# Kernel optimization log

Hardware: AMD Instinct MI355X
Metric: run time of the kernel (lower is better)

Reference implementation:

```python
import jax, jax.numpy as jnp
import numpy as np

N = 4096      # nodes
FEAT = 512    # feature_size
HID = 256     # hidden_dim
E = 131072    # edges (avg degree 32)


def setup_inputs() -> dict:
    key = jax.random.key(0)
    ks = jax.random.split(key, 10)
    x = jax.random.normal(ks[0], (N, FEAT), dtype=jnp.float32)
    edge_index = jax.random.randint(ks[1], (2, E), 0, N)
    edge_attr = jax.random.uniform(ks[2], (E, 1), dtype=jnp.float32)
    # nn.Linear(bias=False) weights, stored as [in, out] so k = x @ Wk
    Wk = jax.random.normal(ks[3], (FEAT, HID), dtype=jnp.float32) / np.sqrt(FEAT)
    Wq = jax.random.normal(ks[4], (FEAT, HID), dtype=jnp.float32) / np.sqrt(FEAT)
    Wv = jax.random.normal(ks[5], (FEAT, FEAT), dtype=jnp.float32) / np.sqrt(FEAT)
    # EmbeddingTable.reset_parameters: normal(0, 1), shape [num_embeddings=2, dim]
    Ek = jax.random.normal(ks[6], (2, HID), dtype=jnp.float32)
    Eq = jax.random.normal(ks[7], (2, HID), dtype=jnp.float32)
    Ev = jax.random.normal(ks[8], (2, FEAT), dtype=jnp.float32)
    # ContinuousEmbeddingIndex params
    idx_bias = jnp.full((1,), 0.5, dtype=jnp.float32)
    idx_mult = jnp.full((1,), 10.0, dtype=jnp.float32)
    return dict(x=x, edge_index=edge_index, edge_attr=edge_attr,
                Wk=Wk, Wq=Wq, Wv=Wv, Ek=Ek, Eq=Eq, Ev=Ev,
                idx_bias=idx_bias, idx_mult=idx_mult)


def reference(x, edge_index, edge_attr, Wk, Wq, Wv, Ek, Eq, Ev, idx_bias, idx_mult):
    n = x.shape[0]
    L = x.shape[-1]  # feature_size, used as softmax scale
    src, dst = edge_index[0], edge_index[1]

    # ContinuousEmbeddingIndex: soft 2-way interpolation weights [E, 2]
    s = jax.nn.sigmoid((edge_attr - idx_bias) * idx_mult)
    w = jnp.concatenate([s, 1.0 - s], axis=-1)

    # per-edge relative embeddings (EmbeddingTable: weights @ embeddings)
    rk = w @ Ek   # [E, HID]
    rq = w @ Eq   # [E, HID]
    rv = w @ Ev   # [E, FEAT]

    k = x @ Wk    # [N, HID]
    q = x @ Wq    # [N, HID]
    v = x @ Wv    # [N, FEAT]

    # A = q k^T + (q_i . Rk_ij) + (k_j . Rq_ij) + q k^T
    # The Rk/Rq terms are nonzero only on edges -> compute per-edge and scatter-add
    # (to_dense_adj sums duplicate edges, matched by .add).
    A = 2.0 * (q @ k.T)                                   # [N, N]
    edge_bias = jnp.sum(q[src] * rk, axis=-1) + jnp.sum(k[dst] * rq, axis=-1)  # [E]
    A = A.at[src, dst].add(edge_bias)
    A = jax.nn.softmax(A / np.sqrt(L), axis=-1)           # dropout = identity (eval)

    # M = A v + sum_j A_ij * Rv_ij  (second term only nonzero on edges)
    M = A @ v
    M = M + jax.ops.segment_sum(A[src, dst][:, None] * rv, src, num_segments=n)
    return M
```

## Files before the change

kernel.cpp:

```cpp
#include <hip/hip_runtime.h>
#include <hip/hip_bf16.h>
#include <cmath>


typedef short bf16x8 __attribute__((ext_vector_type(8)));
typedef float f32x4  __attribute__((ext_vector_type(4)));
typedef unsigned short ushort_t;
typedef unsigned short ushort4v __attribute__((ext_vector_type(4)));
typedef unsigned short ushort8v __attribute__((ext_vector_type(8)));

__device__ __forceinline__ ushort_t f2bf(float f) {
    union { float f; unsigned u; } v; v.f = f;
    unsigned u = v.u;
    u += 0x7FFFu + ((u >> 16) & 1u);
    return (ushort_t)(u >> 16);
}
__device__ __forceinline__ float bf2f(ushort_t h) {
    union { unsigned u; float f; } v; v.u = ((unsigned)h) << 16;
    return v.f;
}
__device__ __forceinline__ void gload_lds16(const void* g, void* l) {
    __builtin_amdgcn_global_load_lds(
        (const __attribute__((address_space(1))) void*)g,
        (__attribute__((address_space(3))) void*)l, 16, 0, 0);
}

__device__ __forceinline__ void gemm_core(
    const ushort_t* __restrict__ A, const ushort_t* __restrict__ B,
    int lda, int ldb, int Ksz, size_t kbase, int bm, int bn,
    ushort_t* As, ushort_t* Bs, f32x4 (&acc)[4][4])
{
    constexpr int BK = 32;
    const int tid  = threadIdx.x;
    const int lane = tid & 63;
    const int wid  = tid >> 6;
    const int wm = (wid >> 1) * 64;
    const int wn = (wid & 1) * 64;

    const int r0 = tid >> 2;
    const int c8 = (tid & 3) * 8;
    const ushort_t* Ag0 = A + (size_t)(bm + r0) * lda + kbase + c8;
    const ushort_t* Bg0 = B + (size_t)(bn + r0) * ldb + kbase + c8;
    const ushort_t* Ag1 = Ag0 + (size_t)64 * lda;
    const ushort_t* Bg1 = Bg0 + (size_t)64 * ldb;
    ushort_t* AsW0 = &As[(wid * 64) * 8];
    ushort_t* AsW1 = &As[(256 + wid * 64) * 8];
    ushort_t* BsW0 = &Bs[(wid * 64) * 8];
    ushort_t* BsW1 = &Bs[(256 + wid * 64) * 8];

    const int fr = lane & 15;
    const int kh = (lane >> 4) * 8;

    for (int k0 = 0; k0 < Ksz; k0 += BK) {
        gload_lds16(Ag0 + k0, AsW0);
        gload_lds16(Ag1 + k0, AsW1);
        gload_lds16(Bg0 + k0, BsW0);
        gload_lds16(Bg1 + k0, BsW1);
        __syncthreads();

        bf16x8 af[4], bfv[4];
        #pragma unroll
        for (int i = 0; i < 4; ++i) {
            af[i]  = *(const bf16x8*)&As[(wm + i * 16 + fr) * 32 + kh];
            bfv[i] = *(const bf16x8*)&Bs[(wn + i * 16 + fr) * 32 + kh];
        }
        #pragma unroll
        for (int i = 0; i < 4; ++i)
            #pragma unroll
            for (int j = 0; j < 4; ++j)
                acc[i][j] = __builtin_amdgcn_mfma_f32_16x16x32_bf16(
                    af[i], bfv[j], acc[i][j], 0, 0, 0);
        __syncthreads();
    }
}

__device__ __forceinline__ int swizzle_bid()
{
    int bid = blockIdx.y * gridDim.x + blockIdx.x;
    const int nwg = gridDim.x * gridDim.y;
    if ((nwg & 7) == 0) {
        const int cpx = nwg >> 3;
        bid = (bid & 7) * cpx + (bid >> 3);
    }
    return bid;
}

template<bool STORE_BF16>
__global__ __launch_bounds__(256) void gemm_nt_mfma(
    const ushort_t* __restrict__ A, const ushort_t* __restrict__ B,
    void* __restrict__ Cv, int lda, int ldb, int ldc, int Ksz, float alpha)
{
    __shared__ ushort_t As[128 * 32];
    __shared__ ushort_t Bs[128 * 32];
    const int bid = swizzle_bid();
    const int bm = (bid / gridDim.x) * 128;
    const int bn = (bid % gridDim.x) * 128;
    f32x4 acc[4][4] = {};
    gemm_core(A, B, lda, ldb, Ksz, 0, bm, bn, As, Bs, acc);

    const int lane = threadIdx.x & 63;
    const int wid  = threadIdx.x >> 6;
    const int wm = (wid >> 1) * 64, wn = (wid & 1) * 64;
    const int cr = (lane >> 4) * 4, cc = lane & 15;
    #pragma unroll
    for (int i = 0; i < 4; ++i)
        #pragma unroll
        for (int j = 0; j < 4; ++j) {
            const int col = bn + wn + j * 16 + cc;
            const int rowb = bm + wm + i * 16 + cr;
            #pragma unroll
            for (int jj = 0; jj < 4; ++jj) {
                const float val = alpha * acc[i][j][jj];
                if (STORE_BF16)
                    ((ushort_t*)Cv)[(size_t)(rowb + jj) * ldc + col] = f2bf(val);
                else
                    ((float*)Cv)[(size_t)(rowb + jj) * ldc + col] = val;
            }
        }
}

__global__ __launch_bounds__(256) void proj_gemm(
    const ushort_t* __restrict__ xb, const ushort_t* __restrict__ Wqkt,
    const ushort_t* __restrict__ Wvt, ushort_t* __restrict__ qkb,
    ushort_t* __restrict__ vTb, int FEAT, int HID, int N)
{
    __shared__ ushort_t As[128 * 32];
    __shared__ ushort_t Bs[128 * 32];
    const int b = blockIdx.x;
    const ushort_t* A; const ushort_t* B; ushort_t* C;
    int bm, bn, ldc;
    if (b < 128) {
        const int gx = (2 * HID) / 128;
        bm = (b / gx) * 128; bn = (b % gx) * 128;
        A = xb; B = Wqkt; C = qkb; ldc = 2 * HID;
    } else {
        const int b2 = b - 128;
        const int gx = N / 128;
        bm = (b2 / gx) * 128; bn = (b2 % gx) * 128;
        A = Wvt; B = xb; C = vTb; ldc = N;
    }
    f32x4 acc[4][4] = {};
    gemm_core(A, B, FEAT, FEAT, FEAT, 0, bm, bn, As, Bs, acc);

    const int lane = threadIdx.x & 63;
    const int wid  = threadIdx.x >> 6;
    const int wm = (wid >> 1) * 64, wn = (wid & 1) * 64;
    const int cr = (lane >> 4) * 4, cc = lane & 15;
    #pragma unroll
    for (int i = 0; i < 4; ++i)
        #pragma unroll
        for (int j = 0; j < 4; ++j) {
            const int col = bn + wn + j * 16 + cc;
            const int rowb = bm + wm + i * 16 + cr;
            #pragma unroll
            for (int jj = 0; jj < 4; ++jj)
                C[(size_t)(rowb + jj) * ldc + col] = f2bf(acc[i][j][jj]);
        }
}

__global__ __launch_bounds__(256) void pv_gemm_splitk(
    const ushort_t* __restrict__ P, const ushort_t* __restrict__ vT,
    ushort_t* __restrict__ parts, int N, int FEAT, int Kchunk)
{
    __shared__ ushort_t As[128 * 32];
    __shared__ ushort_t Bs[128 * 32];
    const int bid = swizzle_bid();
    const int bm = (bid / gridDim.x) * 128;
    const int bn = (bid % gridDim.x) * 128;

    f32x4 acc[4][4] = {};
    gemm_core(P, vT, N, N, Kchunk, (size_t)blockIdx.z * Kchunk, bm, bn, As, Bs, acc);

    const int tid = threadIdx.x;
    const int lane = tid & 63;
    const int wid  = tid >> 6;
    const int wm = (wid >> 1) * 64, wn = (wid & 1) * 64;
    const int cr = (lane >> 4) * 4, cc = lane & 15;
    ushort_t* myPart = parts + (size_t)blockIdx.z * N * FEAT;
    #pragma unroll
    for (int i = 0; i < 4; ++i)
        #pragma unroll
        for (int j = 0; j < 4; ++j) {
            const int col = bn + wn + j * 16 + cc;
            const int rowb = bm + wm + i * 16 + cr;
            #pragma unroll
            for (int jj = 0; jj < 4; ++jj)
                myPart[(size_t)(rowb + jj) * FEAT + col] = f2bf(acc[i][j][jj]);
        }
}

__global__ void reduce_add_rv_kernel(
    const ushort_t* __restrict__ parts, float* __restrict__ out,
    const float* __restrict__ c0, const float* __restrict__ c1,
    const float* __restrict__ Ev, int FEAT, size_t zstride, int nz)
{
    const int i8 = blockIdx.x * 256 + threadIdx.x;
    const int F8 = FEAT / 8;
    const int node = i8 / F8;
    const int f0 = (i8 % F8) * 8;
    float s[8] = {};
    for (int z = 0; z < nz; ++z) {
        const ushort8v p = *(const ushort8v*)(parts + (size_t)z * zstride + (size_t)i8 * 8);
        #pragma unroll
        for (int j = 0; j < 8; ++j) s[j] += bf2f(p[j]);
    }
    const float a0 = c0[node], a1 = c1[node];
    float4 o0, o1;
    const float4 e00 = *(const float4*)(Ev + f0);
    const float4 e01 = *(const float4*)(Ev + f0 + 4);
    const float4 e10 = *(const float4*)(Ev + FEAT + f0);
    const float4 e11 = *(const float4*)(Ev + FEAT + f0 + 4);
    o0.x = s[0] + a0 * e00.x + a1 * e10.x;
    o0.y = s[1] + a0 * e00.y + a1 * e10.y;
    o0.z = s[2] + a0 * e00.z + a1 * e10.z;
    o0.w = s[3] + a0 * e00.w + a1 * e10.w;
    o1.x = s[4] + a0 * e01.x + a1 * e11.x;
    o1.y = s[5] + a0 * e01.y + a1 * e11.y;
    o1.z = s[6] + a0 * e01.z + a1 * e11.z;
    o1.w = s[7] + a0 * e01.w + a1 * e11.w;
    float* op = out + (size_t)node * FEAT + f0;
    *(float4*)op = o0;
    *(float4*)(op + 4) = o1;
}

__global__ __launch_bounds__(256) void prep_kernel(
    const float* __restrict__ x, const float* __restrict__ Wq,
    const float* __restrict__ Wk, const float* __restrict__ Wv,
    ushort_t* __restrict__ xb, ushort_t* __restrict__ Wqkt,
    ushort_t* __restrict__ Wvt, int N, int FEAT, int HID)
{
    const int b = blockIdx.x;
    const int tid = threadIdx.x;
    const int xBlocks = (N * FEAT / 8) / 256;
    if (b < xBlocks) {
        const int i = b * 256 + tid;
        const float4 a = ((const float4*)x)[2 * i];
        const float4 c = ((const float4*)x)[2 * i + 1];
        ushort8v o;
        o[0] = f2bf(a.x); o[1] = f2bf(a.y); o[2] = f2bf(a.z); o[3] = f2bf(a.w);
        o[4] = f2bf(c.x); o[5] = f2bf(c.y); o[6] = f2bf(c.z); o[7] = f2bf(c.w);
        ((ushort8v*)xb)[i] = o;
        return;
    }

    __shared__ float tile[32][33];
    const int qkTiles = (FEAT / 32) * (HID / 32);
    int t = b - xBlocks;
    const float* src; ushort_t* dst; int I, O;
    if (t < qkTiles)            { src = Wq; dst = Wqkt;                       I = FEAT; O = HID; }
    else if (t < 2 * qkTiles)   { src = Wk; dst = Wqkt + (size_t)HID * FEAT;  I = FEAT; O = HID; t -= qkTiles; }
    else                        { src = Wv; dst = Wvt;                        I = FEAT; O = FEAT; t -= 2 * qkTiles; }
    const int ot = O / 32;
    const int r0 = (t / ot) * 32;
    const int c0 = (t % ot) * 32;
    const int lr = tid >> 5;
    const int lc = tid & 31;
    #pragma unroll
    for (int rr = 0; rr < 32; rr += 8)
        tile[lr + rr][lc] = src[(size_t)(r0 + lr + rr) * O + c0 + lc];
    __syncthreads();
    #pragma unroll
    for (int rr = 0; rr < 32; rr += 8)
        dst[(size_t)(c0 + lr + rr) * I + r0 + lc] = f2bf(tile[lc][lr + rr]);
}

__global__ __launch_bounds__(256) void node_dots(
    const ushort_t* __restrict__ qk,
    const float* __restrict__ Ek, const float* __restrict__ Eq,
    float* qk0, float* qk1, float* kq0, float* kq1,
    float* c0, float* c1, int HID)
{
    const int node = blockIdx.x;
    const int t = threadIdx.x;
    const ushort_t* row = qk + (size_t)node * (2 * HID);
    const float qv = bf2f(row[t]);
    const float kv = bf2f(row[HID + t]);
    float p0 = qv * Ek[t];
    float p1 = qv * Ek[HID + t];
    float p2 = kv * Eq[t];
    float p3 = kv * Eq[HID + t];
    #pragma unroll
    for (int off = 32; off > 0; off >>= 1) {
        p0 += __shfl_down(p0, off);
        p1 += __shfl_down(p1, off);
        p2 += __shfl_down(p2, off);
        p3 += __shfl_down(p3, off);
    }
    __shared__ float red[4][4];
    if ((t & 63) == 0) {
        const int w = t >> 6;
        red[w][0] = p0; red[w][1] = p1; red[w][2] = p2; red[w][3] = p3;
    }
    __syncthreads();
    if (t == 0) {
        qk0[node] = red[0][0] + red[1][0] + red[2][0] + red[3][0];
        qk1[node] = red[0][1] + red[1][1] + red[2][1] + red[3][1];
        kq0[node] = red[0][2] + red[1][2] + red[2][2] + red[3][2];
        kq1[node] = red[0][3] + red[1][3] + red[2][3] + red[3][3];
        c0[node] = 0.f;
        c1[node] = 0.f;
    }
}

__global__ void edge_bias_kernel(
    const int* __restrict__ ei, const float* __restrict__ attr,
    const float* __restrict__ qk0, const float* __restrict__ qk1,
    const float* __restrict__ kq0, const float* __restrict__ kq1,
    float* __restrict__ A, int E, int N,
    const float* __restrict__ ibp, const float* __restrict__ imp)
{
    const int e = blockIdx.x * blockDim.x + threadIdx.x;
    if (e >= E) return;
    const int src = ei[e];
    const int dst = ei[E + e];
    const float s = 1.f / (1.f + __expf(-(attr[e] - ibp[0]) * imp[0]));
    const float bias = s * qk0[src] + (1.f - s) * qk1[src]
                     + s * kq0[dst] + (1.f - s) * kq1[dst];
    atomicAdd(&A[(size_t)src * N + dst], bias);
}

__global__ __launch_bounds__(256) void softmax_rows_bf16(
    const float* __restrict__ A, ushort_t* __restrict__ P, int N, float scale)
{
    const int row = blockIdx.x;
    const float* a = A + (size_t)row * N;
    ushort_t* p = P + (size_t)row * N;
    const int t = threadIdx.x;
    float4 vals[4];
    float mx = -1e30f;
    #pragma unroll
    for (int u = 0; u < 4; ++u) {
        float4 vv = ((const float4*)a)[t + u * 256];
        vv.x *= scale; vv.y *= scale; vv.z *= scale; vv.w *= scale;
        vals[u] = vv;
        mx = fmaxf(mx, fmaxf(fmaxf(vv.x, vv.y), fmaxf(vv.z, vv.w)));
    }
    __shared__ float red[4];
    #pragma unroll
    for (int off = 32; off > 0; off >>= 1) mx = fmaxf(mx, __shfl_down(mx, off));
    if ((t & 63) == 0) red[t >> 6] = mx;
    __syncthreads();
    const float m = fmaxf(fmaxf(red[0], red[1]), fmaxf(red[2], red[3]));
    __syncthreads();
    float sum = 0.f;
    #pragma unroll
    for (int u = 0; u < 4; ++u) {
        vals[u].x = __expf(vals[u].x - m);
        vals[u].y = __expf(vals[u].y - m);
        vals[u].z = __expf(vals[u].z - m);
        vals[u].w = __expf(vals[u].w - m);
        sum += vals[u].x + vals[u].y + vals[u].z + vals[u].w;
    }
    #pragma unroll
    for (int off = 32; off > 0; off >>= 1) sum += __shfl_down(sum, off);
    if ((t & 63) == 0) red[t >> 6] = sum;
    __syncthreads();
    const float inv = 1.f / (red[0] + red[1] + red[2] + red[3]);
    #pragma unroll
    for (int u = 0; u < 4; ++u) {
        ushort4v o;
        o[0] = f2bf(vals[u].x * inv);
        o[1] = f2bf(vals[u].y * inv);
        o[2] = f2bf(vals[u].z * inv);
        o[3] = f2bf(vals[u].w * inv);
        ((ushort4v*)p)[t + u * 256] = o;
    }
}

__global__ void edge_coeff_kernel(
    const int* __restrict__ ei, const float* __restrict__ attr,
    const ushort_t* __restrict__ P, float* __restrict__ c0, float* __restrict__ c1,
    int E, int N, const float* __restrict__ ibp, const float* __restrict__ imp)
{
    const int e = blockIdx.x * blockDim.x + threadIdx.x;
    if (e >= E) return;
    const int src = ei[e];
    const int dst = ei[E + e];
    const float s = 1.f / (1.f + __expf(-(attr[e] - ibp[0]) * imp[0]));
    const float pv = bf2f(P[(size_t)src * N + dst]);
    atomicAdd(&c0[src], pv * s);
    atomicAdd(&c1[src], pv * (1.f - s));
}

extern "C" void kernel_launch(void* const* d_in, const int* in_sizes, int n_in,
                              void* d_out, int out_size, void* d_ws, size_t ws_size,
                              hipStream_t stream)
{
    const float* x    = (const float*)d_in[0];
    const int*   ei   = (const int*)d_in[1];
    const float* attr = (const float*)d_in[2];
    const float* Wk   = (const float*)d_in[3];
    const float* Wq   = (const float*)d_in[4];
    const float* Wv   = (const float*)d_in[5];
    const float* Ek   = (const float*)d_in[6];
    const float* Eq   = (const float*)d_in[7];
    const float* Ev   = (const float*)d_in[8];
    const float* ib   = (const float*)d_in[9];
    const float* im   = (const float*)d_in[10];
    float* out = (float*)d_out;

    const int FEAT = (int)lroundf(sqrtf((float)in_sizes[5]));
    const int HID  = in_sizes[3] / FEAT;
    const int N    = in_sizes[0] / FEAT;
    const int E    = in_sizes[2];

    char* w = (char*)d_ws;
    size_t o = 0;
    ushort_t* xb   = (ushort_t*)(w + o); o += (size_t)N * FEAT * 2;
    ushort_t* Wqkt = (ushort_t*)(w + o); o += (size_t)2 * HID * FEAT * 2;
    ushort_t* Wvt  = (ushort_t*)(w + o); o += (size_t)FEAT * FEAT * 2;
    ushort_t* qkb  = (ushort_t*)(w + o); o += (size_t)N * 2 * HID * 2;
    ushort_t* vTb  = (ushort_t*)(w + o); o += (size_t)FEAT * N * 2;
    float*    Abuf = (float*)(w + o);    o += (size_t)N * N * 4;
    ushort_t* Pb   = (ushort_t*)(w + o); o += (size_t)N * N * 2;
    float*    qk0  = (float*)(w + o);    o += (size_t)N * 4;
    float*    qk1  = (float*)(w + o);    o += (size_t)N * 4;
    float*    kq0  = (float*)(w + o);    o += (size_t)N * 4;
    float*    kq1  = (float*)(w + o);    o += (size_t)N * 4;
    float*    c0   = (float*)(w + o);    o += (size_t)N * 4;
    float*    c1   = (float*)(w + o);    o += (size_t)N * 4;
    ushort_t* pvpart = (ushort_t*)Abuf;

    const dim3 blk(256);
    const int NZ = 4;
    const int Kchunk = N / NZ;

    const int xBlocks = (N * FEAT / 8) / 256;
    const int qkTiles = (FEAT / 32) * (HID / 32);
    const int vTiles  = (FEAT / 32) * (FEAT / 32);
    prep_kernel<<<xBlocks + 2 * qkTiles + vTiles, blk, 0, stream>>>(
        x, Wq, Wk, Wv, xb, Wqkt, Wvt, N, FEAT, HID);

    proj_gemm<<<256, blk, 0, stream>>>(xb, Wqkt, Wvt, qkb, vTb, FEAT, HID, N);

    node_dots<<<N, blk, 0, stream>>>(qkb, Ek, Eq, qk0, qk1, kq0, kq1, c0, c1, HID);

    gemm_nt_mfma<false><<<dim3(N / 128, N / 128), blk, 0, stream>>>(
        qkb, qkb + HID, Abuf, 2 * HID, 2 * HID, N, HID, 2.f);

    edge_bias_kernel<<<(E + 255) / 256, blk, 0, stream>>>(ei, attr, qk0, qk1, kq0, kq1,
                                                          Abuf, E, N, ib, im);

    softmax_rows_bf16<<<N, blk, 0, stream>>>(Abuf, Pb, N, 1.f / sqrtf((float)FEAT));

    edge_coeff_kernel<<<(E + 255) / 256, blk, 0, stream>>>(ei, attr, Pb, c0, c1, E, N, ib, im);

    pv_gemm_splitk<<<dim3(FEAT / 128, N / 128, NZ), blk, 0, stream>>>(
        Pb, vTb, pvpart, N, FEAT, Kchunk);

    reduce_add_rv_kernel<<<(N * FEAT / 8) / 256, blk, 0, stream>>>(
        pvpart, out, c0, c1, Ev, FEAT, (size_t)N * FEAT, NZ);
}
```

Before: 130.9 us.

## Store score matrix in fp16 and apply edge biases via CSR in softmax

The QK^T GEMM now writes pre-scaled fp16 scores instead of fp32, halving the N×N intermediate traffic. Edge biases are no longer atomically added into the dense matrix. Instead, edges are bucketed by source row through a count, a single-block scan and a scatter into CSR order, and the softmax kernel adds them into an LDS copy of the row. This trades a few extra small kernels and LDS atomics for fewer global random atomics and less dense read/write bandwidth, at the cost of fp16 precision on the scores.

```diff
diff --git a/kernel.cpp b/kernel.cpp
--- a/kernel.cpp
+++ b/kernel.cpp
@@ -18,6 +18,12 @@
 __device__ __forceinline__ float bf2f(ushort_t h) {
     union { unsigned u; float f; } v; v.u = ((unsigned)h) << 16;
     return v.f;
+}
+__device__ __forceinline__ ushort_t f2h(float f) {
+    union { _Float16 h; ushort_t u; } v; v.h = (_Float16)f; return v.u;
+}
+__device__ __forceinline__ float h2f(ushort_t u) {
+    union { ushort_t u; _Float16 h; } v; v.u = u; return (float)v.h;
 }
 __device__ __forceinline__ void gload_lds16(const void* g, void* l) {
     __builtin_amdgcn_global_load_lds(
@@ -85,7 +91,7 @@
     return bid;
 }
 
-template<bool STORE_BF16>
+template<int MODE>
 __global__ __launch_bounds__(256) void gemm_nt_mfma(
     const ushort_t* __restrict__ A, const ushort_t* __restrict__ B,
     void* __restrict__ Cv, int lda, int ldb, int ldc, int Ksz, float alpha)
@@ -111,10 +117,12 @@
             #pragma unroll
             for (int jj = 0; jj < 4; ++jj) {
                 const float val = alpha * acc[i][j][jj];
-                if (STORE_BF16)
+                if (MODE == 0)
+                    ((float*)Cv)[(size_t)(rowb + jj) * ldc + col] = val;
+                else if (MODE == 1)
                     ((ushort_t*)Cv)[(size_t)(rowb + jj) * ldc + col] = f2bf(val);
                 else
-                    ((float*)Cv)[(size_t)(rowb + jj) * ldc + col] = val;
+                    ((ushort_t*)Cv)[(size_t)(rowb + jj) * ldc + col] = f2h(val);
             }
         }
 }
@@ -122,11 +130,17 @@
 __global__ __launch_bounds__(256) void proj_gemm(
     const ushort_t* __restrict__ xb, const ushort_t* __restrict__ Wqkt,
     const ushort_t* __restrict__ Wvt, ushort_t* __restrict__ qkb,
-    ushort_t* __restrict__ vTb, int FEAT, int HID, int N)
-{
+    ushort_t* __restrict__ vTb, const int* __restrict__ ei,
+    int* __restrict__ rowcnt, int E, int FEAT, int HID, int N)
+{
+    const int b = blockIdx.x;
+    if (b >= 256) {
+        const int e = (b - 256) * 256 + threadIdx.x;
+        if (e < E) atomicAdd(&rowcnt[ei[e]], 1);
+        return;
+    }
     __shared__ ushort_t As[128 * 32];
     __shared__ ushort_t Bs[128 * 32];
-    const int b = blockIdx.x;
     const ushort_t* A; const ushort_t* B; ushort_t* C;
     int bm, bn, ldc;
     if (b < 128) {
@@ -227,11 +241,21 @@
     const float* __restrict__ x, const float* __restrict__ Wq,
     const float* __restrict__ Wk, const float* __restrict__ Wv,
     ushort_t* __restrict__ xb, ushort_t* __restrict__ Wqkt,
-    ushort_t* __restrict__ Wvt, int N, int FEAT, int HID)
+    ushort_t* __restrict__ Wvt, int* __restrict__ rowcnt,
+    int N, int FEAT, int HID)
 {
     const int b = blockIdx.x;
     const int tid = threadIdx.x;
     const int xBlocks = (N * FEAT / 8) / 256;
+    const int qkTiles = (FEAT / 32) * (HID / 32);
+    const int vTiles  = (FEAT / 32) * (FEAT / 32);
+    const int zBase = xBlocks + 2 * qkTiles + vTiles;
+
+    if (b >= zBase) {
+        const int i = (b - zBase) * 256 + tid;
+        if (i < N) rowcnt[i] = 0;
+        return;
+    }
     if (b < xBlocks) {
         const int i = b * 256 + tid;
         const float4 a = ((const float4*)x)[2 * i];
@@ -244,7 +268,6 @@
     }
 
     __shared__ float tile[32][33];
-    const int qkTiles = (FEAT / 32) * (HID / 32);
     int t = b - xBlocks;
     const float* src; ushort_t* dst; int I, O;
     if (t < qkTiles)            { src = Wq; dst = Wqkt;                       I = FEAT; O = HID; }
@@ -302,69 +325,99 @@
     }
 }
 
-__global__ void edge_bias_kernel(
+__global__ __launch_bounds__(256) void scan_kernel(
+    const int* __restrict__ cnt, int* __restrict__ rowptr,
+    int* __restrict__ rowcur, int N)
+{
+    __shared__ int psum[256];
+    const int t = threadIdx.x;
+    const int per = N / 256;
+    int local[16];
+    int base = 0;
+    for (int i = 0; i < per; ++i) { local[i] = base; base += cnt[t * per + i]; }
+    psum[t] = base;
+    __syncthreads();
+    for (int off = 1; off < 256; off <<= 1) {
+        const int v = (t >= off) ? psum[t - off] : 0;
+        __syncthreads();
+        psum[t] += v;
+        __syncthreads();
+    }
+    const int pre = (t == 0) ? 0 : psum[t - 1];
+    for (int i = 0; i < per; ++i) {
+        rowptr[t * per + i] = pre + local[i];
+        rowcur[t * per + i] = pre + local[i];
+    }
+    if (t == 255) rowptr[N] = psum[255];
+}
+
+__global__ void scatter_kernel(
     const int* __restrict__ ei, const float* __restrict__ attr,
     const float* __restrict__ qk0, const float* __restrict__ qk1,
     const float* __restrict__ kq0, const float* __restrict__ kq1,
-    float* __restrict__ A, int E, int N,
+    int* __restrict__ rowcur, int2* __restrict__ ebuf, int E, float scale,
     const float* __restrict__ ibp, const float* __restrict__ imp)
 {
-    const int e = blockIdx.x * blockDim.x + threadIdx.x;
+    const int e = blockIdx.x * 256 + threadIdx.x;
     if (e >= E) return;
     const int src = ei[e];
     const int dst = ei[E + e];
     const float s = 1.f / (1.f + __expf(-(attr[e] - ibp[0]) * imp[0]));
     const float bias = s * qk0[src] + (1.f - s) * qk1[src]
                      + s * kq0[dst] + (1.f - s) * kq1[dst];
-    atomicAdd(&A[(size_t)src * N + dst], bias);
+    const int pos = atomicAdd(&rowcur[src], 1);
+    int2 rec; rec.x = dst; rec.y = __float_as_int(bias * scale);
+    ebuf[pos] = rec;
 }
 
 __global__ __launch_bounds__(256) void softmax_rows_bf16(
-    const float* __restrict__ A, ushort_t* __restrict__ P, int N, float scale)
-{
-    const int row = blockIdx.x;
-    const float* a = A + (size_t)row * N;
-    ushort_t* p = P + (size_t)row * N;
+    const ushort_t* __restrict__ Ah, const int* __restrict__ rowptr,
+    const int2* __restrict__ ebuf, ushort_t* __restrict__ P, int N)
+{
+    __shared__ float row[4096];
+    __shared__ float red[4];
+    const int r = blockIdx.x;
+    const ushort_t* a = Ah + (size_t)r * N;
+    ushort_t* p = P + (size_t)r * N;
     const int t = threadIdx.x;
-    float4 vals[4];
+
+    #pragma unroll
+    for (int u = 0; u < 2; ++u) {
+        const int c = u * 256 + t;
+        const ushort8v hv = ((const ushort8v*)a)[c];
+        #pragma unroll
+        for (int j = 0; j < 8; ++j) row[c * 8 + j] = h2f(hv[j]);
+    }
+    __syncthreads();
+
+    for (int i = rowptr[r] + t; i < rowptr[r + 1]; i += 256) {
+        const int2 rec = ebuf[i];
+        atomicAdd(&row[rec.x], __int_as_float(rec.y));
+    }
+    __syncthreads();
+
     float mx = -1e30f;
-    #pragma unroll
-    for (int u = 0; u < 4; ++u) {
-        float4 vv = ((const float4*)a)[t + u * 256];
-        vv.x *= scale; vv.y *= scale; vv.z *= scale; vv.w *= scale;
-        vals[u] = vv;
-        mx = fmaxf(mx, fmaxf(fmaxf(vv.x, vv.y), fmaxf(vv.z, vv.w)));
-    }
-    __shared__ float red[4];
+    for (int i = t; i < N; i += 256) mx = fmaxf(mx, row[i]);
     #pragma unroll
     for (int off = 32; off > 0; off >>= 1) mx = fmaxf(mx, __shfl_down(mx, off));
     if ((t & 63) == 0) red[t >> 6] = mx;
     __syncthreads();
     const float m = fmaxf(fmaxf(red[0], red[1]), fmaxf(red[2], red[3]));
     __syncthreads();
+
     float sum = 0.f;
-    #pragma unroll
-    for (int u = 0; u < 4; ++u) {
-        vals[u].x = __expf(vals[u].x - m);
-        vals[u].y = __expf(vals[u].y - m);
-        vals[u].z = __expf(vals[u].z - m);
-        vals[u].w = __expf(vals[u].w - m);
-        sum += vals[u].x + vals[u].y + vals[u].z + vals[u].w;
+    for (int i = t; i < N; i += 256) {
+        const float e = __expf(row[i] - m);
+        row[i] = e;
+        sum += e;
     }
     #pragma unroll
     for (int off = 32; off > 0; off >>= 1) sum += __shfl_down(sum, off);
     if ((t & 63) == 0) red[t >> 6] = sum;
     __syncthreads();
     const float inv = 1.f / (red[0] + red[1] + red[2] + red[3]);
-    #pragma unroll
-    for (int u = 0; u < 4; ++u) {
-        ushort4v o;
-        o[0] = f2bf(vals[u].x * inv);
-        o[1] = f2bf(vals[u].y * inv);
-        o[2] = f2bf(vals[u].z * inv);
-        o[3] = f2bf(vals[u].w * inv);
-        ((ushort4v*)p)[t + u * 256] = o;
-    }
+
+    for (int i = t; i < N; i += 256) p[i] = f2bf(row[i] * inv);
 }
 
 __global__ void edge_coeff_kernel(
@@ -411,7 +464,7 @@
     ushort_t* Wvt  = (ushort_t*)(w + o); o += (size_t)FEAT * FEAT * 2;
     ushort_t* qkb  = (ushort_t*)(w + o); o += (size_t)N * 2 * HID * 2;
     ushort_t* vTb  = (ushort_t*)(w + o); o += (size_t)FEAT * N * 2;
-    float*    Abuf = (float*)(w + o);    o += (size_t)N * N * 4;
+    ushort_t* Ah   = (ushort_t*)(w + o); o += (size_t)N * N * 2;
     ushort_t* Pb   = (ushort_t*)(w + o); o += (size_t)N * N * 2;
     float*    qk0  = (float*)(w + o);    o += (size_t)N * 4;
     float*    qk1  = (float*)(w + o);    o += (size_t)N * 4;
@@ -419,29 +472,39 @@
     float*    kq1  = (float*)(w + o);    o += (size_t)N * 4;
     float*    c0   = (float*)(w + o);    o += (size_t)N * 4;
     float*    c1   = (float*)(w + o);    o += (size_t)N * 4;
-    ushort_t* pvpart = (ushort_t*)Abuf;
+    int*      rowcnt = (int*)(w + o);    o += (size_t)N * 4;
+    int*      rowptr = (int*)(w + o);    o += (size_t)(N + 1) * 4;
+    int*      rowcur = (int*)(w + o);    o += (size_t)N * 4;
+    o = (o + 15) & ~(size_t)15;
+    int2*     ebuf   = (int2*)(w + o);   o += (size_t)E * 8;
+    ushort_t* pvpart = Ah;
 
     const dim3 blk(256);
     const int NZ = 4;
     const int Kchunk = N / NZ;
+    const float scale = 1.f / sqrtf((float)FEAT);
 
     const int xBlocks = (N * FEAT / 8) / 256;
     const int qkTiles = (FEAT / 32) * (HID / 32);
     const int vTiles  = (FEAT / 32) * (FEAT / 32);
-    prep_kernel<<<xBlocks + 2 * qkTiles + vTiles, blk, 0, stream>>>(
-        x, Wq, Wk, Wv, xb, Wqkt, Wvt, N, FEAT, HID);
-
-    proj_gemm<<<256, blk, 0, stream>>>(xb, Wqkt, Wvt, qkb, vTb, FEAT, HID, N);
+    const int zBlocks = (N + 255) / 256;
+    prep_kernel<<<xBlocks + 2 * qkTiles + vTiles + zBlocks, blk, 0, stream>>>(
+        x, Wq, Wk, Wv, xb, Wqkt, Wvt, rowcnt, N, FEAT, HID);
+
+    proj_gemm<<<256 + (E + 255) / 256, blk, 0, stream>>>(
+        xb, Wqkt, Wvt, qkb, vTb, ei, rowcnt, E, FEAT, HID, N);
 
     node_dots<<<N, blk, 0, stream>>>(qkb, Ek, Eq, qk0, qk1, kq0, kq1, c0, c1, HID);
 
-    gemm_nt_mfma<false><<<dim3(N / 128, N / 128), blk, 0, stream>>>(
-        qkb, qkb + HID, Abuf, 2 * HID, 2 * HID, N, HID, 2.f);
-
-    edge_bias_kernel<<<(E + 255) / 256, blk, 0, stream>>>(ei, attr, qk0, qk1, kq0, kq1,
-                                                          Abuf, E, N, ib, im);
-
-    softmax_rows_bf16<<<N, blk, 0, stream>>>(Abuf, Pb, N, 1.f / sqrtf((float)FEAT));
+    scan_kernel<<<1, blk, 0, stream>>>(rowcnt, rowptr, rowcur, N);
+
+    scatter_kernel<<<(E + 255) / 256, blk, 0, stream>>>(
+        ei, attr, qk0, qk1, kq0, kq1, rowcur, ebuf, E, scale, ib, im);
+
+    gemm_nt_mfma<2><<<dim3(N / 128, N / 128), blk, 0, stream>>>(
+        qkb, qkb + HID, Ah, 2 * HID, 2 * HID, N, HID, 2.f * scale);
+
+    softmax_rows_bf16<<<N, blk, 0, stream>>>(Ah, rowptr, ebuf, Pb, N);
 
     edge_coeff_kernel<<<(E + 255) / 256, blk, 0, stream>>>(ei, attr, Pb, c0, c1, E, N, ib, im);
 
```

New measurement: 149.3 us. 1.14x slower.
